# Optimization experiments

Measured on AMD Instinct MI355X. Metric: run time of the kernel, lower is better.

## Reference

```python
import jax, jax.numpy as jnp
import numpy as np

N_NODES = 50000
N_EDGES = 800000
D = 128
BN_EPS = 1e-5


def swish(h):
    return h * jax.nn.sigmoid(h)


def linear_bn_swish(h, W, b, g, be):
    # Linear -> BatchNorm1d (training stats, biased var) -> Swish
    h = h @ W + b
    mean = jnp.mean(h, axis=0)
    var = jnp.mean((h - mean) ** 2, axis=0)
    h = (h - mean) * jax.lax.rsqrt(var + BN_EPS) * g + be
    return swish(h)


def setup_inputs() -> dict:
    key = jax.random.key(0)
    ks = jax.random.split(key, 8)
    scale = 1.0 / np.sqrt(D)
    return {
        "x": jax.random.normal(ks[0], (N_NODES, D), dtype=jnp.float32),
        "vals": jax.random.uniform(ks[1], (N_EDGES,), dtype=jnp.float32),
        "W1": jax.random.normal(ks[2], (D, D), dtype=jnp.float32) * scale,
        "b1": jnp.zeros((D,), dtype=jnp.float32),
        "g1": jnp.ones((D,), dtype=jnp.float32),
        "be1": jnp.zeros((D,), dtype=jnp.float32),
        "W2": jax.random.normal(ks[3], (D, D), dtype=jnp.float32) * scale,
        "b2": jnp.zeros((D,), dtype=jnp.float32),
        "g2": jnp.ones((D,), dtype=jnp.float32),
        "be2": jnp.zeros((D,), dtype=jnp.float32),
        "eps": jnp.zeros((1,), dtype=jnp.float32),
        "rows": jax.random.randint(ks[4], (N_EDGES,), 0, N_NODES, dtype=jnp.int32),
        "cols": jax.random.randint(ks[5], (N_EDGES,), 0, N_NODES, dtype=jnp.int32),
    }


def reference(x, vals, W1, b1, g1, be1, W2, b2, g2, be2, eps, rows, cols):
    # out = spmm(adj, x): gather neighbor features, scale by edge weight, scatter-add to rows
    msgs = vals[:, None] * x[cols]                                   # [E, D]
    agg = jax.ops.segment_sum(msgs, rows, num_segments=x.shape[0])   # [N, D]
    h = agg + (1.0 + eps[0]) * x
    h = linear_bn_swish(h, W1, b1, g1, be1)
    h = linear_bn_swish(h, W2, b2, g2, be2)
    return h
```

## Files before the change

### kernel.cpp

```cpp
#include <hip/hip_runtime.h>

#define D 128
#define DH 64
#define BR 64
#define BSH 6
#define NBMAX 1024
#define FCAP 2048
#define GT 512
#define CH 4096
#define SCT 512

typedef float f32x4 __attribute__((ext_vector_type(4)));
typedef short s16x8 __attribute__((ext_vector_type(8)));

static __device__ __forceinline__ unsigned short f2bf(float f) {
    unsigned u = __float_as_uint(f);
    u += 0x7FFF + ((u >> 16) & 1);
    return (unsigned short)(u >> 16);
}
static __device__ __forceinline__ float bflo(unsigned u) { return __uint_as_float(u << 16); }
static __device__ __forceinline__ float bfhi(unsigned u) { return __uint_as_float(u & 0xFFFF0000u); }
static __device__ __forceinline__ float bf2f(short v) {
    return __uint_as_float(((unsigned)(unsigned short)v) << 16);
}

__global__ __launch_bounds__(256)
void k_setup(const float* __restrict__ x, unsigned* __restrict__ xh, int total4,
             const float* __restrict__ W1, const float* __restrict__ W2,
             unsigned short* __restrict__ Wsw1, unsigned short* __restrict__ Wsw2,
             int* __restrict__ ccur, float* __restrict__ stats, int eb) {
    int bid = blockIdx.x, t = threadIdx.x;
    if (bid < eb) {
        int i = bid * 256 + t;
        if (i < total4) {
            float4 v = ((const float4*)x)[i];
            uint2 o;
            o.x = (unsigned)f2bf(v.x) | ((unsigned)f2bf(v.y) << 16);
            o.y = (unsigned)f2bf(v.z) | ((unsigned)f2bf(v.w) << 16);
            ((uint2*)xh)[i] = o;
        }
    } else if (bid < eb + 16) {
        int gidx = (bid - eb) * 256 + t;
        const float* W = (gidx < 2048) ? W1 : W2;
        unsigned short* Wsw = (gidx < 2048) ? Wsw1 : Wsw2;
        int idx = gidx & 2047;
        int lane = idx & 63, nt = (idx >> 6) & 7, kt = idx >> 9;
        int k0 = kt * 32 + (lane >> 4) * 8;
        int n = nt * 16 + (lane & 15);
        unsigned short* dst = &Wsw[(size_t)((kt * 8 + nt) * 64 + lane) * 8];
#pragma unroll
        for (int j = 0; j < 8; ++j) dst[j] = f2bf(W[(k0 + j) * D + n]);
    } else {
        if (t < 512) stats[t] = 0.f;
        for (int i = t; i < NBMAX; i += 256) ccur[i] = 0;
    }
}

__global__ __launch_bounds__(SCT)
void k_cscatter(const int* __restrict__ rows, const int* __restrict__ cols,
                const float* __restrict__ vals, int* __restrict__ gcur,
                uint2* __restrict__ sedge, int E) {
    __shared__ int lcnt[NBMAX];
    __shared__ int lbase[NBMAX];
    __shared__ int gbase[NBMAX];
    __shared__ uint2 sl[CH];
    __shared__ unsigned short sbkt[CH];
    int t = threadIdx.x;
    int base = blockIdx.x * CH;
    int tot = min(E - base, CH);

    for (int i = t; i < NBMAX; i += SCT) lcnt[i] = 0;
    __syncthreads();

    int r[8]; unsigned c[8], v[8];
#pragma unroll
    for (int j = 0; j < 8; ++j) {
        int e = base + j * SCT + t;
        if (e < E) {
            r[j] = rows[e];
            c[j] = (unsigned)cols[e];
            v[j] = __float_as_uint(vals[e]);
            atomicAdd(&lcnt[r[j] >> BSH], 1);
        } else r[j] = -1;
    }
    __syncthreads();

    lbase[t] = lcnt[t];
    lbase[t + SCT] = lcnt[t + SCT];
    __syncthreads();
    for (int d = 1; d < NBMAX; d <<= 1) {
        int a0 = (t >= d) ? lbase[t - d] : 0;
        int i1 = t + SCT;
        int a1 = (i1 >= d) ? lbase[i1 - d] : 0;
        __syncthreads();
        lbase[t] += a0;
        lbase[i1] += a1;
        __syncthreads();
    }
#pragma unroll
    for (int k = 0; k < 2; ++k) {
        int i = t + k * SCT;
        int cnt = lcnt[i];
        gbase[i] = cnt ? atomicAdd(&gcur[i], cnt) : 0;
        lbase[i] -= cnt;
    }
    __syncthreads();
    for (int i = t; i < NBMAX; i += SCT) lcnt[i] = 0;
    __syncthreads();

#pragma unroll
    for (int j = 0; j < 8; ++j) {
        if (r[j] >= 0) {
            int b = r[j] >> BSH;
            int p = lbase[b] + atomicAdd(&lcnt[b], 1);
            sl[p] = make_uint2(c[j] | ((unsigned)(r[j] & (BR - 1)) << 16), v[j]);
            sbkt[p] = (unsigned short)b;
        }
    }
    __syncthreads();

#pragma unroll
    for (int j = 0; j < 8; ++j) {
        int i = j * SCT + t;
        if (i < tot) {
            int b = sbkt[i];
            int pos = gbase[b] + (i - lbase[b]);
            if (pos < FCAP) sedge[(size_t)b * FCAP + pos] = sl[i];
        }
    }
}

__global__ __launch_bounds__(GT, 8)
void k_sortgather(const uint2* __restrict__ sedge, const int* __restrict__ ccur,
                  const unsigned* __restrict__ xh, const float* __restrict__ eps,
                  unsigned* __restrict__ aggh, int N) {
    __shared__ int cnt[BR], sbase[BR], cur[BR];
    __shared__ uint2 ebufA[FCAP];
    __shared__ uint2 ebufB[FCAP];
    int b = blockIdx.x, t = threadIdx.x;
    size_t e0 = (size_t)b * FCAP;
    int cntE = ccur[b];
    if (cntE > FCAP) cntE = FCAP;
    if (t < BR) { cnt[t] = 0; cur[t] = 0; }
    __syncthreads();
    for (int i = t; i < cntE; i += GT) {
        uint2 ed = sedge[e0 + i];
        ebufA[i] = ed;
        atomicAdd(&cnt[ed.x >> 16], 1);
    }
    __syncthreads();
    if (t < BR) sbase[t] = cnt[t];
    __syncthreads();
    for (int d = 1; d < BR; d <<= 1) {
        int add = (t < BR && t >= d) ? sbase[t - d] : 0;
        __syncthreads();
        if (t < BR) sbase[t] += add;
        __syncthreads();
    }
    if (t < BR) sbase[t] -= cnt[t];
    __syncthreads();
    for (int i = t; i < cntE; i += GT) {
        uint2 ed = ebufA[i];
        int r = ed.x >> 16;
        int p = sbase[r] + atomicAdd(&cur[r], 1);
        ebufB[p] = make_uint2(ed.x & 0xFFFFu, ed.y);
    }
    __syncthreads();

    int lane = t & 63, w = t >> 6;
    float s = 1.0f + eps[0];
    int row0 = b * BR;
    for (int rl = w; rl < BR; rl += 8) {
        int grow = row0 + rl;
        if (grow >= N) break;
        unsigned u = xh[(size_t)grow * DH + lane];
        float ax = s * bflo(u), ay = s * bfhi(u);
        int i = sbase[rl];
        int i1 = (rl < BR - 1) ? sbase[rl + 1] : cntE;
        for (; i + 8 <= i1; i += 8) {
            uint2 ed[8];
            unsigned uu[8];
#pragma unroll
            for (int j = 0; j < 8; ++j) ed[j] = ebufB[i + j];
#pragma unroll
            for (int j = 0; j < 8; ++j) uu[j] = xh[(size_t)ed[j].x * DH + lane];
#pragma unroll
            for (int j = 0; j < 8; ++j) {
                float v = __uint_as_float(ed[j].y);
                ax += v * bflo(uu[j]);
                ay += v * bfhi(uu[j]);
            }
        }
        for (; i < i1; ++i) {
            uint2 ed = ebufB[i];
            unsigned uu = xh[(size_t)ed.x * DH + lane];
            float v = __uint_as_float(ed.y);
            ax += v * bflo(uu);
            ay += v * bfhi(uu);
        }
        aggh[(size_t)grow * DH + lane] = (unsigned)f2bf(ax) | ((unsigned)f2bf(ay) << 16);
    }
}

__global__ __launch_bounds__(256)
void k_gemm(const unsigned short* __restrict__ A, const unsigned short* __restrict__ Wsw,
            const float* __restrict__ bias, unsigned short* __restrict__ Hout,
            float* __restrict__ stats, int N) {
    __shared__ float redS[4 * D];
    __shared__ float redQ[4 * D];
    int tid = threadIdx.x, lane = tid & 63, w = tid >> 6;
    int row0 = blockIdx.x * 64 + w * 16;
    int m = lane & 15, quad = lane >> 4;

    f32x4 acc[8];
#pragma unroll
    for (int nt = 0; nt < 8; ++nt) acc[nt] = (f32x4){0.f, 0.f, 0.f, 0.f};

    int arow = row0 + m;
    bool avalid = arow < N;
    const s16x8* wp = (const s16x8*)Wsw;
    s16x8 az = {0, 0, 0, 0, 0, 0, 0, 0};
#pragma unroll
    for (int kt = 0; kt < 4; ++kt) {
        s16x8 a = avalid ? *(const s16x8*)&A[(size_t)arow * D + kt * 32 + quad * 8] : az;
#pragma unroll
        for (int nt = 0; nt < 8; ++nt) {
            s16x8 b = wp[(kt * 8 + nt) * 64 + lane];
            acc[nt] = __builtin_amdgcn_mfma_f32_16x16x32_bf16(a, b, acc[nt], 0, 0, 0);
        }
    }

#pragma unroll
    for (int nt = 0; nt < 8; ++nt) {
        float bv = bias[nt * 16 + m];
        float s = 0.f, q = 0.f;
#pragma unroll
        for (int r = 0; r < 4; ++r) {
            int row = row0 + quad * 4 + r;
            float h = acc[nt][r] + bv;
            if (row < N) {
                Hout[(size_t)row * D + nt * 16 + m] = f2bf(h);
                s += h; q += h * h;
            }
        }
        s += __shfl_xor(s, 16, 64); s += __shfl_xor(s, 32, 64);
        q += __shfl_xor(q, 16, 64); q += __shfl_xor(q, 32, 64);
        if (quad == 0) {
            redS[w * D + nt * 16 + m] = s;
            redQ[w * D + nt * 16 + m] = q;
        }
    }
    __syncthreads();
    if (tid < D) {
        float ts = redS[tid] + redS[D + tid] + redS[2 * D + tid] + redS[3 * D + tid];
        float tq = redQ[tid] + redQ[D + tid] + redQ[2 * D + tid] + redQ[3 * D + tid];
        atomicAdd(&stats[tid], ts);
        atomicAdd(&stats[D + tid], tq);
    }
}

__global__ __launch_bounds__(256)
void k_gemm2f(const unsigned short* __restrict__ H1, const unsigned short* __restrict__ Wsw,
              const float* __restrict__ bias, const float* __restrict__ stats1,
              const float* __restrict__ g1, const float* __restrict__ be1, float invN,
              unsigned short* __restrict__ Hout, float* __restrict__ stats2, int N) {
    __shared__ float redS[4 * D];
    __shared__ float redQ[4 * D];
    __shared__ float sa[D], sb[D];
    int tid = threadIdx.x, lane = tid & 63, w = tid >> 6;
    if (tid < D) {
        float mean = stats1[tid] * invN;
        float var = fmaxf(stats1[D + tid] * invN - mean * mean, 0.f);
        float a = g1[tid] * rsqrtf(var + 1e-5f);
        sa[tid] = a;
        sb[tid] = be1[tid] - mean * a;
    }
    __syncthreads();

    int row0 = blockIdx.x * 64 + w * 16;
    int m = lane & 15, quad = lane >> 4;

    f32x4 acc[8];
#pragma unroll
    for (int nt = 0; nt < 8; ++nt) acc[nt] = (f32x4){0.f, 0.f, 0.f, 0.f};

    int arow = row0 + m;
    bool avalid = arow < N;
    const s16x8* wp = (const s16x8*)Wsw;
    s16x8 az = {0, 0, 0, 0, 0, 0, 0, 0};
#pragma unroll
    for (int kt = 0; kt < 4; ++kt) {
        s16x8 a = az;
        if (avalid) {
            s16x8 raw = *(const s16x8*)&H1[(size_t)arow * D + kt * 32 + quad * 8];
#pragma unroll
            for (int j = 0; j < 8; ++j) {
                int k = kt * 32 + quad * 8 + j;
                float dd = bf2f(raw[j]) * sa[k] + sb[k];
                float o = dd / (1.f + __expf(-dd));
                a[j] = (short)f2bf(o);
            }
        }
#pragma unroll
        for (int nt = 0; nt < 8; ++nt) {
            s16x8 b = wp[(kt * 8 + nt) * 64 + lane];
            acc[nt] = __builtin_amdgcn_mfma_f32_16x16x32_bf16(a, b, acc[nt], 0, 0, 0);
        }
    }

#pragma unroll
    for (int nt = 0; nt < 8; ++nt) {
        float bv = bias[nt * 16 + m];
        float s = 0.f, q = 0.f;
#pragma unroll
        for (int r = 0; r < 4; ++r) {
            int row = row0 + quad * 4 + r;
            float h = acc[nt][r] + bv;
            if (row < N) {
                Hout[(size_t)row * D + nt * 16 + m] = f2bf(h);
                s += h; q += h * h;
            }
        }
        s += __shfl_xor(s, 16, 64); s += __shfl_xor(s, 32, 64);
        q += __shfl_xor(q, 16, 64); q += __shfl_xor(q, 32, 64);
        if (quad == 0) {
            redS[w * D + nt * 16 + m] = s;
            redQ[w * D + nt * 16 + m] = q;
        }
    }
    __syncthreads();
    if (tid < D) {
        float ts = redS[tid] + redS[D + tid] + redS[2 * D + tid] + redS[3 * D + tid];
        float tq = redQ[tid] + redQ[D + tid] + redQ[2 * D + tid] + redQ[3 * D + tid];
        atomicAdd(&stats2[tid], ts);
        atomicAdd(&stats2[D + tid], tq);
    }
}

__global__ void k_bnswish(const unsigned* __restrict__ inh, float* __restrict__ outp,
                          const float* __restrict__ stats, const float* __restrict__ g,
                          const float* __restrict__ be, float invN, int total4) {
    __shared__ float sa[D], sb[D];
    int j = threadIdx.x;
    if (j < D) {
        float mean = stats[j] * invN;
        float var = fmaxf(stats[D + j] * invN - mean * mean, 0.f);
        float a = g[j] * rsqrtf(var + 1e-5f);
        sa[j] = a;
        sb[j] = be[j] - mean * a;
    }
    __syncthreads();
    int i = blockIdx.x * blockDim.x + threadIdx.x;
    if (i >= total4) return;
    uint2 u = ((const uint2*)inh)[i];
    int c = (i * 4) & (D - 1);
    float d0 = bflo(u.x) * sa[c + 0] + sb[c + 0];
    float d1 = bfhi(u.x) * sa[c + 1] + sb[c + 1];
    float d2 = bflo(u.y) * sa[c + 2] + sb[c + 2];
    float d3 = bfhi(u.y) * sa[c + 3] + sb[c + 3];
    float o0 = d0 / (1.f + __expf(-d0));
    float o1 = d1 / (1.f + __expf(-d1));
    float o2 = d2 / (1.f + __expf(-d2));
    float o3 = d3 / (1.f + __expf(-d3));
    ((float4*)outp)[i] = make_float4(o0, o1, o2, o3);
}

extern "C" void kernel_launch(void* const* d_in, const int* in_sizes, int n_in,
                              void* d_out, int out_size, void* d_ws, size_t ws_size,
                              hipStream_t stream) {
    const float* x    = (const float*)d_in[0];
    const float* vals = (const float*)d_in[1];
    const float* W1   = (const float*)d_in[2];
    const float* b1   = (const float*)d_in[3];
    const float* g1   = (const float*)d_in[4];
    const float* be1  = (const float*)d_in[5];
    const float* W2   = (const float*)d_in[6];
    const float* b2   = (const float*)d_in[7];
    const float* g2   = (const float*)d_in[8];
    const float* be2  = (const float*)d_in[9];
    const float* eps  = (const float*)d_in[10];
    const int*  rows  = (const int*)d_in[11];
    const int*  cols  = (const int*)d_in[12];
    float* out = (float*)d_out;

    int N = in_sizes[0] / D;
    int E = in_sizes[1];
    int nb = (N + BR - 1) / BR;

    char* p = (char*)d_ws;
    float* stats = (float*)p;              p += 4 * D * sizeof(float);
    int* ccur = (int*)p;                   p += (size_t)NBMAX * sizeof(int);
    p = (char*)(((uintptr_t)p + 15) & ~(uintptr_t)15);
    unsigned short* Wsw1 = (unsigned short*)p; p += (size_t)D * D * 2;
    unsigned short* Wsw2 = (unsigned short*)p; p += (size_t)D * D * 2;
    p = (char*)(((uintptr_t)p + 15) & ~(uintptr_t)15);
    uint2* sedge  = (uint2*)p;             p += (size_t)nb * FCAP * sizeof(uint2);
    unsigned* xh = (unsigned*)p;           p += (size_t)N * DH * sizeof(unsigned);
    unsigned* aggh = (unsigned*)p;

    float* stats1 = stats;
    float* stats2 = stats + 2 * D;

    int total4 = N * D / 4;
    int eb = (total4 + 255) / 256;
    int gblk = (N + 63) / 64;
    float invN = 1.0f / (float)N;
    int scb = (E + CH - 1) / CH;

    k_setup<<<eb + 17, 256, 0, stream>>>(x, xh, total4, W1, W2, Wsw1, Wsw2,
                                         ccur, stats, eb);
    k_cscatter<<<scb, SCT, 0, stream>>>(rows, cols, vals, ccur, sedge, E);
    k_sortgather<<<nb, GT, 0, stream>>>(sedge, ccur, xh, eps, aggh, N);
    k_gemm<<<gblk, 256, 0, stream>>>((const unsigned short*)aggh, Wsw1, b1,
                                     (unsigned short*)xh, stats1, N);
    k_gemm2f<<<gblk, 256, 0, stream>>>((const unsigned short*)xh, Wsw2, b2,
                                       stats1, g1, be1, invN,
                                       (unsigned short*)aggh, stats2, N);
    k_bnswish<<<eb, 256, 0, stream>>>(aggh, out, stats2, g2, be2, invN, total4);
}
```

Before: 221.8 us.

## Fuse sparse aggregation with first GEMM through a shared-memory tile

The gather/aggregate kernel now writes each block's 64 aggregated bf16 rows into a padded LDS tile instead of global memory. The block then runs the first 128x128 MFMA GEMM on that tile, with 8 waves split as 4 row groups by 2 column halves, and accumulates the BN1 stats in the same kernel. This drops one kernel launch and the global write and re-read of the aggregate buffer. In exchange, GEMM work is added to a kernel that already uses a lot of LDS, which may lower occupancy, and the edge buffer shares its memory with the tile.

```diff
diff --git a/kernel.cpp b/kernel.cpp
--- a/kernel.cpp
+++ b/kernel.cpp
@@ -9,6 +9,7 @@
 #define GT 512
 #define CH 4096
 #define SCT 512
+#define TS 68
 
 typedef float f32x4 __attribute__((ext_vector_type(4)));
 typedef short s16x8 __attribute__((ext_vector_type(8)));
@@ -131,12 +132,18 @@
 }
 
 __global__ __launch_bounds__(GT, 8)
-void k_sortgather(const uint2* __restrict__ sedge, const int* __restrict__ ccur,
-                  const unsigned* __restrict__ xh, const float* __restrict__ eps,
-                  unsigned* __restrict__ aggh, int N) {
+void k_sgg(const uint2* __restrict__ sedge, const int* __restrict__ ccur,
+           const unsigned* __restrict__ xh, const float* __restrict__ eps,
+           const unsigned short* __restrict__ Wsw, const float* __restrict__ bias,
+           unsigned short* __restrict__ Hout, float* __restrict__ stats, int N) {
     __shared__ int cnt[BR], sbase[BR], cur[BR];
-    __shared__ uint2 ebufA[FCAP];
+    __shared__ __align__(16) unsigned char uAbuf[64 * TS * 4];
     __shared__ uint2 ebufB[FCAP];
+    __shared__ float redS[8 * 64];
+    __shared__ float redQ[8 * 64];
+    uint2* ebufA = (uint2*)uAbuf;
+    unsigned* tile = (unsigned*)uAbuf;
+
     int b = blockIdx.x, t = threadIdx.x;
     size_t e0 = (size_t)b * FCAP;
     int cntE = ccur[b];
@@ -172,7 +179,7 @@
     int row0 = b * BR;
     for (int rl = w; rl < BR; rl += 8) {
         int grow = row0 + rl;
-        if (grow >= N) break;
+        if (grow >= N) { tile[rl * TS + lane] = 0; continue; }
         unsigned u = xh[(size_t)grow * DH + lane];
         float ax = s * bflo(u), ay = s * bfhi(u);
         int i = sbase[rl];
@@ -198,64 +205,62 @@
             ax += v * bflo(uu);
             ay += v * bfhi(uu);
         }
-        aggh[(size_t)grow * DH + lane] = (unsigned)f2bf(ax) | ((unsigned)f2bf(ay) << 16);
-    }
-}
-
-__global__ __launch_bounds__(256)
-void k_gemm(const unsigned short* __restrict__ A, const unsigned short* __restrict__ Wsw,
-            const float* __restrict__ bias, unsigned short* __restrict__ Hout,
-            float* __restrict__ stats, int N) {
-    __shared__ float redS[4 * D];
-    __shared__ float redQ[4 * D];
-    int tid = threadIdx.x, lane = tid & 63, w = tid >> 6;
-    int row0 = blockIdx.x * 64 + w * 16;
+        tile[rl * TS + lane] = (unsigned)f2bf(ax) | ((unsigned)f2bf(ay) << 16);
+    }
+    __syncthreads();
+
     int m = lane & 15, quad = lane >> 4;
-
-    f32x4 acc[8];
-#pragma unroll
-    for (int nt = 0; nt < 8; ++nt) acc[nt] = (f32x4){0.f, 0.f, 0.f, 0.f};
-
-    int arow = row0 + m;
-    bool avalid = arow < N;
+    int wr = w & 3, wc = w >> 2;
+    int arowl = wr * 16 + m;
+
+    f32x4 acc[4];
+#pragma unroll
+    for (int ntl = 0; ntl < 4; ++ntl) acc[ntl] = (f32x4){0.f, 0.f, 0.f, 0.f};
+
     const s16x8* wp = (const s16x8*)Wsw;
-    s16x8 az = {0, 0, 0, 0, 0, 0, 0, 0};
 #pragma unroll
     for (int kt = 0; kt < 4; ++kt) {
-        s16x8 a = avalid ? *(const s16x8*)&A[(size_t)arow * D + kt * 32 + quad * 8] : az;
-#pragma unroll
-        for (int nt = 0; nt < 8; ++nt) {
-            s16x8 b = wp[(kt * 8 + nt) * 64 + lane];
-            acc[nt] = __builtin_amdgcn_mfma_f32_16x16x32_bf16(a, b, acc[nt], 0, 0, 0);
-        }
-    }
-
-#pragma unroll
-    for (int nt = 0; nt < 8; ++nt) {
+        s16x8 a = *(const s16x8*)&tile[arowl * TS + kt * 16 + quad * 4];
+#pragma unroll
+        for (int ntl = 0; ntl < 4; ++ntl) {
+            int nt = wc * 4 + ntl;
+            s16x8 bf = wp[(kt * 8 + nt) * 64 + lane];
+            acc[ntl] = __builtin_amdgcn_mfma_f32_16x16x32_bf16(a, bf, acc[ntl], 0, 0, 0);
+        }
+    }
+
+#pragma unroll
+    for (int ntl = 0; ntl < 4; ++ntl) {
+        int nt = wc * 4 + ntl;
         float bv = bias[nt * 16 + m];
-        float s = 0.f, q = 0.f;
+        float ss = 0.f, q = 0.f;
 #pragma unroll
         for (int r = 0; r < 4; ++r) {
-            int row = row0 + quad * 4 + r;
-            float h = acc[nt][r] + bv;
+            int row = row0 + wr * 16 + quad * 4 + r;
+            float h = acc[ntl][r] + bv;
             if (row < N) {
                 Hout[(size_t)row * D + nt * 16 + m] = f2bf(h);
-                s += h; q += h * h;
+                ss += h; q += h * h;
             }
         }
-        s += __shfl_xor(s, 16, 64); s += __shfl_xor(s, 32, 64);
-        q += __shfl_xor(q, 16, 64); q += __shfl_xor(q, 32, 64);
+        ss += __shfl_xor(ss, 16, 64); ss += __shfl_xor(ss, 32, 64);
+        q += __shfl_xor(q, 16, 64);   q += __shfl_xor(q, 32, 64);
         if (quad == 0) {
-            redS[w * D + nt * 16 + m] = s;
-            redQ[w * D + nt * 16 + m] = q;
-        }
-    }
-    __syncthreads();
-    if (tid < D) {
-        float ts = redS[tid] + redS[D + tid] + redS[2 * D + tid] + redS[3 * D + tid];
-        float tq = redQ[tid] + redQ[D + tid] + redQ[2 * D + tid] + redQ[3 * D + tid];
-        atomicAdd(&stats[tid], ts);
-        atomicAdd(&stats[D + tid], tq);
+            redS[w * 64 + ntl * 16 + m] = ss;
+            redQ[w * 64 + ntl * 16 + m] = q;
+        }
+    }
+    __syncthreads();
+    if (t < D) {
+        int ch = t >> 6, cl = t & 63;
+        float ts = 0.f, tq = 0.f;
+#pragma unroll
+        for (int wr2 = 0; wr2 < 4; ++wr2) {
+            ts += redS[(ch * 4 + wr2) * 64 + cl];
+            tq += redQ[(ch * 4 + wr2) * 64 + cl];
+        }
+        atomicAdd(&stats[t], ts);
+        atomicAdd(&stats[D + t], tq);
     }
 }
 
@@ -396,7 +401,7 @@
     p = (char*)(((uintptr_t)p + 15) & ~(uintptr_t)15);
     uint2* sedge  = (uint2*)p;             p += (size_t)nb * FCAP * sizeof(uint2);
     unsigned* xh = (unsigned*)p;           p += (size_t)N * DH * sizeof(unsigned);
-    unsigned* aggh = (unsigned*)p;
+    unsigned* h1 = (unsigned*)p;
 
     float* stats1 = stats;
     float* stats2 = stats + 2 * D;
@@ -410,11 +415,10 @@
     k_setup<<<eb + 17, 256, 0, stream>>>(x, xh, total4, W1, W2, Wsw1, Wsw2,
                                          ccur, stats, eb);
     k_cscatter<<<scb, SCT, 0, stream>>>(rows, cols, vals, ccur, sedge, E);
-    k_sortgather<<<nb, GT, 0, stream>>>(sedge, ccur, xh, eps, aggh, N);
-    k_gemm<<<gblk, 256, 0, stream>>>((const unsigned short*)aggh, Wsw1, b1,
-                                     (unsigned short*)xh, stats1, N);
-    k_gemm2f<<<gblk, 256, 0, stream>>>((const unsigned short*)xh, Wsw2, b2,
+    k_sgg<<<nb, GT, 0, stream>>>(sedge, ccur, xh, eps, Wsw1, b1,
+                                 (unsigned short*)h1, stats1, N);
+    k_gemm2f<<<gblk, 256, 0, stream>>>((const unsigned short*)h1, Wsw2, b2,
                                        stats1, g1, be1, invN,
-                                       (unsigned short*)aggh, stats2, N);
-    k_bnswish<<<eb, 256, 0, stream>>>(aggh, out, stats2, g2, be2, invN, total4);
-}
+                                       (unsigned short*)xh, stats2, N);
+    k_bnswish<<<eb, 256, 0, stream>>>(xh, out, stats2, g2, be2, invN, total4);
+}
```

Result: faster. 210.2 us (median of 3 runs) (-5.2%).
